# Kernel optimization log

Hardware: AMD Instinct MI355X
Metric: run time of the kernel (lower is better)

## Reference

```python
import jax, jax.numpy as jnp
import numpy as np

B, H, W, C = 4, 64, 64, 96
EXPAND = 2
D_INNER = EXPAND * C  # 192
N = 16   # d_state
K = 4    # scan directions
DT_RANK = int(np.ceil(C / 16))  # 6


def setup_inputs() -> dict:
    key = jax.random.key(0)
    ks = jax.random.split(key, 8)
    def rn(k, shape, scale=0.02):
        return jax.random.normal(k, shape, dtype=jnp.float32) * scale
    return {
        "x": jax.random.normal(ks[0], (B, H, W, C), dtype=jnp.float32),
        "ln_g": jnp.ones((C,), jnp.float32),
        "ln_b": jnp.zeros((C,), jnp.float32),
        "in_proj_w": rn(ks[1], (C, 2 * D_INNER)),
        "in_proj_b": jnp.zeros((2 * D_INNER,), jnp.float32),
        "conv_w": rn(ks[2], (D_INNER, 1, 3, 3), 0.1),
        "conv_b": jnp.zeros((D_INNER,), jnp.float32),
        "x_proj_w": rn(ks[3], (K, DT_RANK + 2 * N, D_INNER)),
        "dt_proj_w": rn(ks[4], (K, D_INNER, DT_RANK), 0.1),
        "dt_proj_b": rn(ks[5], (K, D_INNER), 0.1),
        "A_logs": jnp.log(jnp.tile(jnp.arange(1, N + 1, dtype=jnp.float32)[None, :], (K * D_INNER, 1))),
        "Ds": jnp.ones((K * D_INNER,), jnp.float32),
        "out_norm_g": jnp.ones((D_INNER,), jnp.float32),
        "out_norm_b": jnp.zeros((D_INNER,), jnp.float32),
        "out_proj_w": rn(ks[6], (D_INNER, C)),
        "out_proj_b": jnp.zeros((C,), jnp.float32),
    }


def _ln(x, g, b, eps):
    mu = x.mean(-1, keepdims=True)
    var = jnp.mean((x - mu) ** 2, axis=-1, keepdims=True)
    return (x - mu) * jax.lax.rsqrt(var + eps) * g + b


def _vss_forward(x, ln_g, ln_b, in_proj_w, in_proj_b, conv_w, conv_b,
                 x_proj_w, dt_proj_w, dt_proj_b, A_logs, Ds,
                 out_norm_g, out_norm_b, out_proj_w, out_proj_b):
    Bb, Hh, Ww, Cc = x.shape
    L = Hh * Ww
    d = D_INNER
    # ln_1 (eps=1e-6), then SS2D on channels-first layout
    xn = _ln(x, ln_g, ln_b, 1e-6)
    xz = jnp.einsum('bhwc,ce->bhwe', xn, in_proj_w) + in_proj_b
    xi, z = jnp.split(xz, 2, axis=-1)
    xi = xi.transpose(0, 3, 1, 2)  # (B, d, H, W)
    xi = jax.lax.conv_general_dilated(
        xi, conv_w, (1, 1), 'SAME', feature_group_count=d,
        dimension_numbers=('NCHW', 'OIHW', 'NCHW'))
    xi = jax.nn.silu(xi + conv_b[None, :, None, None])
    # 4 scan directions: row-major, col-major, and their reverses
    x_hw = xi.reshape(Bb, d, L)
    x_wh = xi.transpose(0, 1, 3, 2).reshape(Bb, d, L)
    xs = jnp.stack([x_hw, x_wh], axis=1)                      # (B,2,d,L)
    xs = jnp.concatenate([xs, jnp.flip(xs, axis=-1)], axis=1)  # (B,K,d,L)
    x_dbl = jnp.einsum('bkdl,kcd->bkcl', xs, x_proj_w)         # (B,K,R+2N,L)
    dt_r = x_dbl[:, :, :DT_RANK]
    Bs = x_dbl[:, :, DT_RANK:DT_RANK + N]                      # (B,K,N,L)
    Cs = x_dbl[:, :, DT_RANK + N:]                             # (B,K,N,L)
    dts = jnp.einsum('bkrl,kdr->bkdl', dt_r, dt_proj_w)
    dts = jax.nn.softplus(dts + dt_proj_b[None, :, :, None])
    A = -jnp.exp(A_logs).reshape(K, d, N)
    Dsk = Ds.reshape(K, d)

    def step(h, inp):
        u_t, dt_t, B_t, C_t = inp                  # (B,K,d),(B,K,d),(B,K,N),(B,K,N)
        dA = jnp.exp(dt_t[..., None] * A)          # (B,K,d,N)
        h = dA * h + (dt_t * u_t)[..., None] * B_t[:, :, None, :]
        y = jnp.einsum('bkdn,bkn->bkd', h, C_t)
        return h, y

    seq = (xs.transpose(3, 0, 1, 2), dts.transpose(3, 0, 1, 2),
           Bs.transpose(3, 0, 1, 2), Cs.transpose(3, 0, 1, 2))
    h0 = jnp.zeros((Bb, K, d, N), xs.dtype)
    _, ys = jax.lax.scan(step, h0, seq)            # ys: (L,B,K,d)
    ys = ys.transpose(1, 2, 3, 0)                  # (B,K,d,L)
    ys = ys + Dsk[None, :, :, None] * xs
    # merge the 4 directions back into one row-major map
    inv_y = jnp.flip(ys[:, 2:4], axis=-1)
    wh_y = ys[:, 1].reshape(Bb, d, Ww, Hh).transpose(0, 1, 3, 2).reshape(Bb, d, L)
    invwh_y = inv_y[:, 1].reshape(Bb, d, Ww, Hh).transpose(0, 1, 3, 2).reshape(Bb, d, L)
    y = ys[:, 0] + inv_y[:, 0] + wh_y + invwh_y    # (B,d,L)
    y = y.transpose(0, 2, 1).reshape(Bb, Hh, Ww, d)
    y = _ln(y, out_norm_g, out_norm_b, 1e-5)
    y = y * jax.nn.silu(z)
    out = jnp.einsum('bhwd,dc->bhwc', y, out_proj_w) + out_proj_b
    return x + out  # residual (drop_path = 0 -> identity)


def reference(x, ln_g, ln_b, in_proj_w, in_proj_b, conv_w, conv_b, x_proj_w,
              dt_proj_w, dt_proj_b, A_logs, Ds, out_norm_g, out_norm_b,
              out_proj_w, out_proj_b):
    return _vss_forward(x, ln_g, ln_b, in_proj_w, in_proj_b, conv_w, conv_b,
                        x_proj_w, dt_proj_w, dt_proj_b, A_logs, Ds,
                        out_norm_g, out_norm_b, out_proj_w, out_proj_b)
```

## Files before the change

kernel.cpp:

```cpp
#include <hip/hip_runtime.h>
#include <math.h>

#define CC   96
#define DIN  192
#define NST  16
#define KDIR 4
#define DTR  6
#define LL   4096
#define BB   4
#define NSEG 128
#define SEGLEN 32
#define XROW 40

#define SZ_BLD ((long)BB*LL*DIN)

__device__ __forceinline__ float sigmoidf_(float x){
    return __builtin_amdgcn_rcpf(1.0f + __expf(-x));
}
__device__ __forceinline__ int whmap(int l){ return ((l & 63) << 6) | (l >> 6); }
__device__ __forceinline__ int mapk(int k, int l){
    switch(k & 3){
        case 0:  return l;
        case 1:  return whmap(l);
        case 2:  return LL - 1 - l;
        default: return whmap(LL - 1 - l);
    }
}

__device__ __forceinline__ void dt_and_E(float s, float& dt, float& E){
    const float LOG2E = 1.4426950408889634f;
    const float LN2   = 0.6931471805599453f;
    float sn  = s * LOG2E;
    float t   = __builtin_amdgcn_exp2f(-fabsf(sn));
    float opt = 1.0f + t;
    float r   = __builtin_amdgcn_rcpf(opt);
    E  = (s > 0.f) ? t*r : r;
    dt = LN2 * (fmaxf(sn, 0.f) + __builtin_amdgcn_logf(opt));
}
__device__ __forceinline__ void pow_tree(float E, float* En){
    En[0]=E;
    float E2=E*E;        En[1]=E2;
    En[2]=E2*E;  float E4=E2*E2; En[3]=E4;
    En[4]=E4*E;  En[5]=E4*E2;  En[6]=E4*En[2];
    float E8=E4*E4;      En[7]=E8;
    En[8]=E8*E;  En[9]=E8*E2;  En[10]=E8*En[2]; En[11]=E8*E4;
    En[12]=E8*En[4]; En[13]=E8*En[5]; En[14]=E8*En[6]; En[15]=E8*E8;
}
__device__ __forceinline__ void dir_base(int k, int lg0, int& p0, int& stride){
    switch(k & 3){
        case 0:  p0 = lg0;               stride = 1;   break;
        case 1:  p0 = whmap(lg0);        stride = 64;  break;
        case 2:  p0 = LL - 1 - lg0;      stride = -1;  break;
        default: p0 = whmap(LL-1-lg0);   stride = -64; break;
    }
}

__global__ __launch_bounds__(384) void kA(const float* __restrict__ x,
        const float* __restrict__ lng, const float* __restrict__ lnb,
        const float* __restrict__ W,   const float* __restrict__ bias,
        float* __restrict__ xi, float* __restrict__ z)
{
    __shared__ float xn[16*96];
    __shared__ float sc1[384], sc2[384];
    __shared__ float mu[16], rs[16];
    int t = threadIdx.x;
    long row0 = (long)blockIdx.x * 16;

    for(int q=t; q<16*96; q+=384) xn[q] = x[row0*96 + q];
    __syncthreads();
    {
        int r = t/24, i = t%24;
        float s=0.f, ss=0.f;
        #pragma unroll
        for(int j=0;j<4;j++){ float v = xn[r*96 + i + j*24]; s+=v; ss+=v*v; }
        sc1[t]=s; sc2[t]=ss;
        __syncthreads();
        if(t<16){
            float S=0.f, SS=0.f;
            for(int j=0;j<24;j++){ S+=sc1[t*24+j]; SS+=sc2[t*24+j]; }
            float m = S*(1.0f/96.0f);
            float var = SS*(1.0f/96.0f) - m*m;
            mu[t]=m; rs[t]=rsqrtf(var + 1e-6f);
        }
        __syncthreads();
    }
    for(int q=t; q<16*96; q+=384){
        int r=q/96, c=q%96;
        xn[q] = (xn[q]-mu[r])*rs[r]*lng[c] + lnb[c];
    }
    __syncthreads();

    float acc[16];
    #pragma unroll
    for(int r=0;r<16;r++) acc[r]=0.f;
    for(int c=0;c<96;c++){
        float wv = W[c*384 + t];
        #pragma unroll
        for(int r=0;r<16;r++) acc[r] = fmaf(xn[r*96+c], wv, acc[r]);
    }
    float bv = bias[t];
    if(t < 192){
        for(int r=0;r<16;r++) xi[(row0+r)*DIN + t] = acc[r] + bv;
    } else {
        int e = t - 192;
        for(int r=0;r<16;r++) z[(row0+r)*DIN + e] = acc[r] + bv;
    }
}

__global__ __launch_bounds__(256) void kB(const float* __restrict__ xi,
        const float* __restrict__ cw, const float* __restrict__ cb,
        float* __restrict__ xc)
{
    long idx = (long)blockIdx.x*256 + threadIdx.x;
    if(idx >= SZ_BLD) return;
    int d = (int)(idx % DIN);
    long rg = idx / DIN;
    int p = (int)(rg % LL); int b = (int)(rg / LL);
    int h = p >> 6, w = p & 63;
    float acc = 0.f;
    #pragma unroll
    for(int dh=0; dh<3; dh++){
        int hh = h + dh - 1;
        if(hh < 0 || hh >= 64) continue;
        #pragma unroll
        for(int dw=0; dw<3; dw++){
            int ww2 = w + dw - 1;
            if(ww2 < 0 || ww2 >= 64) continue;
            acc = fmaf(xi[((long)b*LL + hh*64 + ww2)*DIN + d], cw[d*9 + dh*3 + dw], acc);
        }
    }
    acc += cb[d];
    xc[idx] = acc * sigmoidf_(acc);
}

__global__ __launch_bounds__(192) void kC(const float* __restrict__ xc,
        const float* __restrict__ xw, float* __restrict__ xdbl)
{
    __shared__ float ls[16*192];
    int t = threadIdx.x;
    long row0 = (long)blockIdx.x * 16;
    int b  = (int)(row0 / LL);
    int p0 = (int)(row0 % LL);
    for(int q=t; q<16*192; q+=192) ls[q] = xc[row0*DIN + q];
    __syncthreads();
    if(t < 152){
        int k = t/38, c = t%38;
        const float* wr = xw + (long)(k*38 + c)*192;
        float acc[16];
        #pragma unroll
        for(int r=0;r<16;r++) acc[r]=0.f;
        for(int d=0; d<192; d+=4){
            float4 wv = *(const float4*)(wr + d);
            #pragma unroll
            for(int r=0;r<16;r++){
                float4 lv = *(const float4*)(&ls[r*192 + d]);
                acc[r] = fmaf(lv.x,wv.x, fmaf(lv.y,wv.y, fmaf(lv.z,wv.z, fmaf(lv.w,wv.w, acc[r]))));
            }
        }
        int cs = (c < 6) ? c : c + 2;
        for(int r=0;r<16;r++){
            int p = p0 + r;
            int lk;
            if(k==0) lk = p;
            else if(k==1) lk = whmap(p);
            else if(k==2) lk = LL-1-p;
            else lk = LL-1-whmap(p);
            xdbl[(((long)(b*KDIR + k)*LL + lk)*XROW) + cs] = acc[r];
        }
    }
}

__global__ __launch_bounds__(192) void kD2(const float* __restrict__ xc,
        const float* __restrict__ xdbl, const float* __restrict__ alog,
        const float* __restrict__ dtw,  const float* __restrict__ dtb,
        float* __restrict__ hend, float* __restrict__ dtsum)
{
    __shared__ float rows[SEGLEN*XROW];
    int t = threadIdx.x;
    int blk = blockIdx.x;
    int bk = blk / NSEG, seg = blk % NSEG;
    int b = bk / KDIR, k = bk % KDIR;
    {
        const float* src = xdbl + ((long)bk*LL + seg*SEGLEN)*XROW;
        for(int q=t; q<SEGLEN*XROW; q+=192) rows[q] = src[q];
    }
    int d = t, kd = k*192 + d;
    float a[16]; bool fast = true;
    #pragma unroll
    for(int n=0;n<16;n++){
        a[n] = -__expf(alog[kd*16 + n]);
        fast = fast && (fabsf(a[n] + (float)(n+1)) < 1e-3f);
    }
    float w6[6];
    #pragma unroll
    for(int r=0;r<6;r++) w6[r] = dtw[kd*6 + r];
    float bdt = dtb[kd];

    int lg0 = seg * SEGLEN;
    int p0, stride; dir_base(k, lg0, p0, stride);
    long addr  = ((long)b*LL + p0)*DIN + d;
    long astep = (long)stride*DIN;

    float h[16];
    #pragma unroll
    for(int n=0;n<16;n++) h[n]=0.f;
    float sdt = 0.f;
    __syncthreads();

    float u = xc[addr];
    for(int i=0; i<SEGLEN; i++){
        const float* row = &rows[i*XROW];
        float s = bdt;
        #pragma unroll
        for(int r=0;r<6;r++) s = fmaf(row[r], w6[r], s);
        float dt, E; dt_and_E(s, dt, E);
        sdt += dt;
        float wi = dt * u;
        float unext = 0.f;
        long addrN = addr + astep;
        if(i+1 < SEGLEN) unext = xc[addrN];
        float En[16];
        if(fast){ pow_tree(E, En); }
        else {
            #pragma unroll
            for(int n=0;n<16;n++) En[n] = __expf(dt * a[n]);
        }
        float Bv[16];
        #pragma unroll
        for(int n=0;n<16;n+=4) *(float4*)(Bv+n) = *(const float4*)(row + 8 + n);
        #pragma unroll
        for(int n=0;n<16;n++) h[n] = fmaf(En[n], h[n], wi*Bv[n]);
        addr = addrN; u = unext;
    }
    long hb = (((long)bk*NSEG + seg)*192 + d)*16;
    #pragma unroll
    for(int n=0;n<16;n+=4)
        *(float4*)(&hend[hb+n]) = make_float4(h[n],h[n+1],h[n+2],h[n+3]);
    dtsum[((long)bk*NSEG + seg)*192 + d] = sdt;
}

__global__ __launch_bounds__(256) void kE2(const float* __restrict__ alog,
        const float* __restrict__ dtsum, float* __restrict__ hx)
{
    int bk = blockIdx.x;
    int k = bk & 3;
    int t = threadIdx.x;
    float an[12], H[12];
    #pragma unroll
    for(int j=0;j<12;j++){
        int sidx = j*256 + t;
        int d = sidx >> 4, n = sidx & 15;
        an[j] = -__expf(alog[(k*192 + d)*16 + n]);
        H[j] = 0.f;
    }
    long hbase = (long)bk*NSEG*3072;
    long sbase = (long)bk*NSEG*192;
    float he[12], sd[12];
    #pragma unroll
    for(int j=0;j<12;j++){
        he[j] = hx[hbase + j*256 + t];
        sd[j] = dtsum[sbase + ((j*256 + t) >> 4)];
    }
    for(int seg=0; seg<NSEG; seg++){
        float heN[12], sdN[12];
        if(seg+1 < NSEG){
            long h2 = hbase + (long)(seg+1)*3072;
            long s2 = sbase + (long)(seg+1)*192;
            #pragma unroll
            for(int j=0;j<12;j++){
                heN[j] = hx[h2 + j*256 + t];
                sdN[j] = dtsum[s2 + ((j*256 + t) >> 4)];
            }
        } else {
            #pragma unroll
            for(int j=0;j<12;j++){ heN[j]=0.f; sdN[j]=0.f; }
        }
        long h1 = hbase + (long)seg*3072;
        #pragma unroll
        for(int j=0;j<12;j++){
            float P = __expf(an[j]*sd[j]);
            hx[h1 + j*256 + t] = H[j];
            H[j] = fmaf(P, H[j], he[j]);
        }
        #pragma unroll
        for(int j=0;j<12;j++){ he[j]=heN[j]; sd[j]=sdN[j]; }
    }
}

__global__ __launch_bounds__(192) void kF2(const float* __restrict__ xc,
        const float* __restrict__ xdbl, const float* __restrict__ alog,
        const float* __restrict__ dtw,  const float* __restrict__ dtb,
        const float* __restrict__ Ds,   const float* __restrict__ Hprev,
        float* __restrict__ ys0, float* __restrict__ ys123)
{
    __shared__ float rows[SEGLEN*XROW];
    int t = threadIdx.x;
    int blk = blockIdx.x;
    int bk = blk / NSEG, seg = blk % NSEG;
    int b = bk / KDIR, k = bk % KDIR;
    {
        const float* src = xdbl + ((long)bk*LL + seg*SEGLEN)*XROW;
        for(int q=t; q<SEGLEN*XROW; q+=192) rows[q] = src[q];
    }
    int d = t, kd = k*192 + d;
    float a[16]; bool fast = true;
    #pragma unroll
    for(int n=0;n<16;n++){
        a[n] = -__expf(alog[kd*16 + n]);
        fast = fast && (fabsf(a[n] + (float)(n+1)) < 1e-3f);
    }
    float w6[6];
    #pragma unroll
    for(int r=0;r<6;r++) w6[r] = dtw[kd*6 + r];
    float bdt = dtb[kd];
    float Dd  = Ds[kd];
    float h[16];
    long hb = (((long)bk*NSEG + seg)*192 + d)*16;
    #pragma unroll
    for(int n=0;n<16;n+=4){
        float4 v = *(const float4*)(&Hprev[hb+n]);
        h[n]=v.x; h[n+1]=v.y; h[n+2]=v.z; h[n+3]=v.w;
    }
    float* ybuf = (k==0) ? ys0 : (ys123 + (long)(k-1)*SZ_BLD);

    int lg0 = seg * SEGLEN;
    int p0, stride; dir_base(k, lg0, p0, stride);
    long addr  = ((long)b*LL + p0)*DIN + d;
    long astep = (long)stride*DIN;
    __syncthreads();

    float u = xc[addr];
    for(int i=0; i<SEGLEN; i++){
        const float* row = &rows[i*XROW];
        float s = bdt;
        #pragma unroll
        for(int r=0;r<6;r++) s = fmaf(row[r], w6[r], s);
        float dt, E; dt_and_E(s, dt, E);
        float wi = dt * u;
        float unext = 0.f;
        long addrN = addr + astep;
        if(i+1 < SEGLEN) unext = xc[addrN];
        float En[16];
        if(fast){ pow_tree(E, En); }
        else {
            #pragma unroll
            for(int n=0;n<16;n++) En[n] = __expf(dt * a[n]);
        }
        float Bv[16], Cv[16];
        #pragma unroll
        for(int n=0;n<16;n+=4){
            *(float4*)(Bv+n) = *(const float4*)(row + 8 + n);
            *(float4*)(Cv+n) = *(const float4*)(row + 24 + n);
        }
        float y = Dd * u;
        #pragma unroll
        for(int n=0;n<16;n++){
            h[n] = fmaf(En[n], h[n], wi*Bv[n]);
            y = fmaf(h[n], Cv[n], y);
        }
        ybuf[addr] = y;
        addr = addrN; u = unext;
    }
}

__global__ __launch_bounds__(384) void kG(const float* __restrict__ ys0,
        const float* __restrict__ ys123, const float* __restrict__ z,
        const float* __restrict__ ong, const float* __restrict__ onb,
        const float* __restrict__ Wout, const float* __restrict__ ob,
        const float* __restrict__ x, float* __restrict__ out)
{
    __shared__ float yb[16*192];
    __shared__ float sc1[384], sc2[384];
    __shared__ float mu[16], rs[16];
    int t = threadIdx.x;
    long row0 = (long)blockIdx.x * 16;

    for(int q=t; q<3072; q+=384){
        long off = row0*DIN + q;
        yb[q] = ys0[off] + ys123[off] + ys123[SZ_BLD + off] + ys123[2*SZ_BLD + off];
    }
    __syncthreads();
    {
        int r = t/24, i = t%24;
        float s=0.f, ss=0.f;
        #pragma unroll
        for(int j=0;j<8;j++){ float v = yb[r*192 + i*8 + j]; s+=v; ss+=v*v; }
        sc1[t]=s; sc2[t]=ss;
        __syncthreads();
        if(t<16){
            float S=0.f, SS=0.f;
            for(int j=0;j<24;j++){ S+=sc1[t*24+j]; SS+=sc2[t*24+j]; }
            float m = S*(1.0f/192.0f);
            float var = SS*(1.0f/192.0f) - m*m;
            mu[t]=m; rs[t]=rsqrtf(var + 1e-5f);
        }
        __syncthreads();
    }
    for(int q=t; q<3072; q+=384){
        int r=q/192, dd=q%192;
        float v = (yb[q]-mu[r])*rs[r]*ong[dd] + onb[dd];
        float zz = z[row0*DIN + q];
        yb[q] = v * (zz * sigmoidf_(zz));
    }
    __syncthreads();
    int c = t % 96, rg4 = t / 96;
    float acc[4] = {0.f,0.f,0.f,0.f};
    for(int dd=0; dd<192; dd++){
        float wv = Wout[dd*96 + c];
        #pragma unroll
        for(int j=0;j<4;j++) acc[j] = fmaf(yb[(rg4*4+j)*192 + dd], wv, acc[j]);
    }
    float bv = ob[c];
    for(int j=0;j<4;j++){
        long row = row0 + rg4*4 + j;
        out[row*96 + c] = x[row*96 + c] + acc[j] + bv;
    }
}

extern "C" void kernel_launch(void* const* d_in, const int* in_sizes, int n_in,
                              void* d_out, int out_size, void* d_ws, size_t ws_size,
                              hipStream_t stream)
{
    const float* x    = (const float*)d_in[0];
    const float* lng  = (const float*)d_in[1];
    const float* lnb  = (const float*)d_in[2];
    const float* ipw  = (const float*)d_in[3];
    const float* ipb  = (const float*)d_in[4];
    const float* cw   = (const float*)d_in[5];
    const float* cb   = (const float*)d_in[6];
    const float* xpw  = (const float*)d_in[7];
    const float* dtw  = (const float*)d_in[8];
    const float* dtb  = (const float*)d_in[9];
    const float* alog = (const float*)d_in[10];
    const float* Ds   = (const float*)d_in[11];
    const float* ong  = (const float*)d_in[12];
    const float* onb  = (const float*)d_in[13];
    const float* opw  = (const float*)d_in[14];
    const float* opb  = (const float*)d_in[15];

    float* ws    = (float*)d_ws;
    float* xi    = ws + 0;
    float* z     = ws + 3145728;
    float* xc    = ws + 6291456;
    float* xdbl  = ws + 9437184;
    float* ys123 = ws + 12058624;
    float* hx    = ws + 21495808;
    float* dtsum = ws + 27787264;
    float* ys0   = xi;
    float* out   = (float*)d_out;

    hipLaunchKernelGGL(kA,  dim3(1024),  dim3(384), 0, stream, x, lng, lnb, ipw, ipb, xi, z);
    hipLaunchKernelGGL(kB,  dim3(12288), dim3(256), 0, stream, xi, cw, cb, xc);
    hipLaunchKernelGGL(kC,  dim3(1024),  dim3(192), 0, stream, xc, xpw, xdbl);
    hipLaunchKernelGGL(kD2, dim3(2048),  dim3(192), 0, stream, xc, xdbl, alog, dtw, dtb,
                       hx, dtsum);
    hipLaunchKernelGGL(kE2, dim3(16),    dim3(256), 0, stream, alog, dtsum, hx);
    hipLaunchKernelGGL(kF2, dim3(2048),  dim3(192), 0, stream, xc, xdbl, alog, dtw, dtb,
                       Ds, hx, ys0, ys123);
    hipLaunchKernelGGL(kG,  dim3(1024),  dim3(384), 0, stream, ys0, ys123, z, ong, onb,
                       opw, opb, x, out);
}
```

Before: 351.2 us.

## Parallelize inter-segment state carry with a warp-shuffle scan

Replaces the sequential carry kernel, which used 16 blocks each walking 128 segments in order, with a version that assigns 16 lanes per (bk,d,n) chain. Each lane composes 8 segments locally, then the lanes run a Hillis-Steele scan with shuffles and write the exclusive prefix states. The kernel launches 3072 blocks instead of 16, so the GPU is filled and the serial dependency chain gets much shorter. In exchange, the global accesses become strided (192 and 3072 element strides per lane), and the unused mapk helper is dropped.

```diff
diff --git a/kernel.cpp b/kernel.cpp
--- a/kernel.cpp
+++ b/kernel.cpp
@@ -18,14 +18,6 @@
     return __builtin_amdgcn_rcpf(1.0f + __expf(-x));
 }
 __device__ __forceinline__ int whmap(int l){ return ((l & 63) << 6) | (l >> 6); }
-__device__ __forceinline__ int mapk(int k, int l){
-    switch(k & 3){
-        case 0:  return l;
-        case 1:  return whmap(l);
-        case 2:  return LL - 1 - l;
-        default: return whmap(LL - 1 - l);
-    }
-}
 
 __device__ __forceinline__ void dt_and_E(float s, float& dt, float& E){
     const float LOG2E = 1.4426950408889634f;
@@ -239,51 +231,49 @@
     dtsum[((long)bk*NSEG + seg)*192 + d] = sdt;
 }
 
-__global__ __launch_bounds__(256) void kE2(const float* __restrict__ alog,
+__global__ __launch_bounds__(256) void kE3(const float* __restrict__ alog,
         const float* __restrict__ dtsum, float* __restrict__ hx)
 {
-    int bk = blockIdx.x;
-    int k = bk & 3;
-    int t = threadIdx.x;
-    float an[12], H[12];
-    #pragma unroll
-    for(int j=0;j<12;j++){
-        int sidx = j*256 + t;
-        int d = sidx >> 4, n = sidx & 15;
-        an[j] = -__expf(alog[(k*192 + d)*16 + n]);
-        H[j] = 0.f;
-    }
-    long hbase = (long)bk*NSEG*3072;
-    long sbase = (long)bk*NSEG*192;
-    float he[12], sd[12];
-    #pragma unroll
-    for(int j=0;j<12;j++){
-        he[j] = hx[hbase + j*256 + t];
-        sd[j] = dtsum[sbase + ((j*256 + t) >> 4)];
-    }
-    for(int seg=0; seg<NSEG; seg++){
-        float heN[12], sdN[12];
-        if(seg+1 < NSEG){
-            long h2 = hbase + (long)(seg+1)*3072;
-            long s2 = sbase + (long)(seg+1)*192;
-            #pragma unroll
-            for(int j=0;j<12;j++){
-                heN[j] = hx[h2 + j*256 + t];
-                sdN[j] = dtsum[s2 + ((j*256 + t) >> 4)];
-            }
-        } else {
-            #pragma unroll
-            for(int j=0;j<12;j++){ heN[j]=0.f; sdN[j]=0.f; }
-        }
-        long h1 = hbase + (long)seg*3072;
-        #pragma unroll
-        for(int j=0;j<12;j++){
-            float P = __expf(an[j]*sd[j]);
-            hx[h1 + j*256 + t] = H[j];
-            H[j] = fmaf(P, H[j], he[j]);
-        }
-        #pragma unroll
-        for(int j=0;j<12;j++){ he[j]=heN[j]; sd[j]=sdN[j]; }
+    int tid = blockIdx.x*256 + threadIdx.x;
+    int c     = tid & 15;
+    int chain = tid >> 4;
+    int n  = chain & 15;
+    int d  = (chain >> 4) % 192;
+    int bk = chain / 3072;
+    int k  = bk & 3;
+    float an = -__expf(alog[(k*192 + d)*16 + n]);
+    long sbase = (long)bk*NSEG*192  + d;
+    long hbase = (long)bk*NSEG*3072 + d*16 + n;
+    int seg0 = c*8;
+
+    float P[8], he[8];
+    #pragma unroll
+    for(int i=0;i<8;i++){
+        float sd = dtsum[sbase + (long)(seg0+i)*192];
+        he[i]    = hx[hbase + (long)(seg0+i)*3072];
+        P[i]     = __expf(an * sd);
+    }
+    float Pc = 1.f, Hc = 0.f;
+    #pragma unroll
+    for(int i=0;i<8;i++){
+        Hc = fmaf(P[i], Hc, he[i]);
+        Pc *= P[i];
+    }
+    #pragma unroll
+    for(int dist=1; dist<16; dist<<=1){
+        float Pp = __shfl_up(Pc, dist, 16);
+        float Hp = __shfl_up(Hc, dist, 16);
+        if(c >= dist){
+            Hc = fmaf(Pc, Hp, Hc);
+            Pc *= Pp;
+        }
+    }
+    float H = __shfl_up(Hc, 1, 16);
+    if(c == 0) H = 0.f;
+    #pragma unroll
+    for(int i=0;i<8;i++){
+        hx[hbase + (long)(seg0+i)*3072] = H;
+        H = fmaf(P[i], H, he[i]);
     }
 }
 
@@ -454,7 +444,7 @@
     hipLaunchKernelGGL(kC,  dim3(1024),  dim3(192), 0, stream, xc, xpw, xdbl);
     hipLaunchKernelGGL(kD2, dim3(2048),  dim3(192), 0, stream, xc, xdbl, alog, dtw, dtb,
                        hx, dtsum);
-    hipLaunchKernelGGL(kE2, dim3(16),    dim3(256), 0, stream, alog, dtsum, hx);
+    hipLaunchKernelGGL(kE3, dim3(3072),  dim3(256), 0, stream, alog, dtsum, hx);
     hipLaunchKernelGGL(kF2, dim3(2048),  dim3(192), 0, stream, xc, xdbl, alog, dtw, dtb,
                        Ds, hx, ys0, ys123);
     hipLaunchKernelGGL(kG,  dim3(1024),  dim3(384), 0, stream, ys0, ys123, z, ong, onb,
```

Measured after the change: 314.3 us. -10.5%, faster.
